# Performance work log

Measured on AMD Instinct MI355X. Metric: run time of the kernel, lower is better.

Reference implementation:

```python
import jax, jax.numpy as jnp
import numpy as np

NUM_NEIGHBORS = 9  # cfg['num_neighbors']


def _cdist(a, b):
    """Euclidean cdist. a: [..., M, D], b: [..., N, D] -> [..., M, N]."""
    a2 = jnp.sum(a * a, axis=-1)[..., :, None]
    b2 = jnp.sum(b * b, axis=-1)[..., None, :]
    ab = jnp.einsum('...md,...nd->...mn', a, b)
    return jnp.sqrt(jnp.maximum(a2 + b2 - 2.0 * ab, 0.0))


def setup_inputs() -> dict:
    key = jax.random.key(0)
    k1, k2 = jax.random.split(key)
    B, P, D, N = 8, 784, 384, 16384
    embedding = jax.random.normal(k1, (B * P, D), dtype=jnp.float32)
    embedding_coreset = jax.random.normal(k2, (N, D), dtype=jnp.float32)
    return {"embedding": embedding, "embedding_coreset": embedding_coreset, "batch_size": B}


def reference(embedding, embedding_coreset, batch_size):
    D = embedding.shape[-1]
    # 1-NN of every patch against the coreset
    dists = _cdist(embedding, embedding_coreset)          # [B*P, N]
    patch_scores = jnp.min(dists, axis=1).reshape(batch_size, -1)   # [B, P]
    locations = jnp.argmin(dists, axis=1).reshape(batch_size, -1)   # [B, P]

    b = jnp.arange(batch_size)
    max_patches = jnp.argmax(patch_scores, axis=1)        # [B]
    emb = embedding.reshape(batch_size, -1, D)            # [B, P, D]
    max_feats = emb[b, max_patches]                       # [B, D]
    score = patch_scores[b, max_patches]                  # [B]
    nn_index = locations[b, max_patches]                  # [B]
    nn_sample = embedding_coreset[nn_index]               # [B, D]

    # k-NN of the nearest coreset sample within the coreset (support set)
    d_nn = _cdist(nn_sample, embedding_coreset)           # [B, N]
    _, support = jax.lax.top_k(-d_nn, NUM_NEIGHBORS)      # smallest dists, ascending -> [B, K]
    support_feats = embedding_coreset[support]            # [B, K, D]

    # distances from max patch feature to the support samples
    d_sup = _cdist(max_feats[:, None, :], support_feats)[:, 0, :]  # [B, K]
    weights = (1.0 - jax.nn.softmax(d_sup, axis=1))[:, 0]          # [B]
    return weights * score
```

## Files before the change

kernel.cpp:

```cpp
#include <hip/hip_runtime.h>
#include <hip/hip_bf16.h>
#include <math.h>

#define M_TOTAL 6272
#define N_CS    16384
#define D_DIM   384
#define BATCH   8
#define P_PATCH 784
#define KNN     9

#define MTILES  (M_TOTAL / 128)
#define NTILES2 (N_CS / 256)

typedef _Float16 half8 __attribute__((ext_vector_type(8)));
typedef float    floatx4 __attribute__((ext_vector_type(4)));

__device__ __forceinline__ void async_copy16(const void* g, void* l) {
    __builtin_amdgcn_global_load_lds(
        (const __attribute__((address_space(1))) void*)g,
        (__attribute__((address_space(3))) void*)l, 16, 0, 0);
}

__global__ void convert_all_kernel(const float* __restrict__ emb,
                                   const float* __restrict__ cs,
                                   _Float16* __restrict__ embh,
                                   _Float16* __restrict__ csh,
                                   float* __restrict__ cnorm) {
    int w = threadIdx.x >> 6, lane = threadIdx.x & 63;
    int row = blockIdx.x * 4 + w;
    if (row >= N_CS + M_TOTAL) return;
    bool is_cs = row < N_CS;
    const float* r = (is_cs ? cs + (size_t)row * D_DIM
                            : emb + (size_t)(row - N_CS) * D_DIM) + lane * 6;
    float2 a = *(const float2*)r;
    float2 b = *(const float2*)(r + 2);
    float2 c = *(const float2*)(r + 4);
    union { _Float16 h[2]; unsigned u; } p0, p1, p2;
    p0.h[0] = (_Float16)a.x; p0.h[1] = (_Float16)a.y;
    p1.h[0] = (_Float16)b.x; p1.h[1] = (_Float16)b.y;
    p2.h[0] = (_Float16)c.x; p2.h[1] = (_Float16)c.y;
    unsigned* dst = (unsigned*)(is_cs ? csh + (size_t)row * D_DIM
                                      : embh + (size_t)(row - N_CS) * D_DIM) + lane * 3;
    dst[0] = p0.u; dst[1] = p1.u; dst[2] = p2.u;
    if (is_cs) {
        float s = a.x * a.x + a.y * a.y + b.x * b.x + b.y * b.y + c.x * c.x + c.y * c.y;
#pragma unroll
        for (int mk = 1; mk <= 32; mk <<= 1) s += __shfl_xor(s, mk, 64);
        if (lane == 0) cnorm[row] = s;
    }
}

__global__ __launch_bounds__(256, 2) void mindist_mfma_kernel(
    const _Float16* __restrict__ embh, const _Float16* __restrict__ csh,
    const float* __restrict__ cnorm,
    float* __restrict__ pvals, int* __restrict__ pidx) {
    __shared__ _Float16 As[128 * 64];
    __shared__ _Float16 Bs[256 * 64];

    const int tid  = threadIdx.x;
    const int lane = tid & 63;
    const int w    = tid >> 6;
    const int wr   = w >> 1, wc = w & 1;
    const int row0  = blockIdx.x * 128;
    const int cbase = blockIdx.y * 256;
    const int q   = lane >> 4;
    const int cl  = lane & 15;
    const int cl7 = cl & 7;

    floatx4 acc[4][8];
#pragma unroll
    for (int mi = 0; mi < 4; ++mi)
#pragma unroll
        for (int nj = 0; nj < 8; ++nj) acc[mi][nj] = (floatx4){0.f, 0.f, 0.f, 0.f};

    float cn_l[8];
#pragma unroll
    for (int nj = 0; nj < 8; ++nj)
        cn_l[nj] = cnorm[cbase + wc * 128 + nj * 16 + cl];

    const int sub = lane >> 3;
    const int gch = (lane & 7) ^ sub;
    const int kb  = gch * 8;

    for (int kk = 0; kk < D_DIM; kk += 64) {
        __syncthreads();
#pragma unroll
        for (int i = 0; i < 12; ++i) {
            int inst = w * 12 + i;
            if (inst < 16) {
                int r = inst * 8 + sub;
                async_copy16(embh + (size_t)(row0 + r) * D_DIM + kk + kb,
                             &As[inst * 512 + lane * 8]);
            } else {
                int blk = inst - 16;
                int r = blk * 8 + sub;
                async_copy16(csh + (size_t)(cbase + r) * D_DIM + kk + kb,
                             &Bs[blk * 512 + lane * 8]);
            }
        }
        __syncthreads();
#pragma unroll
        for (int ks = 0; ks < 64; ks += 32) {
            const int ks8 = ks >> 3;
            half8 af[4], bf[8];
#pragma unroll
            for (int mi = 0; mi < 4; ++mi)
                af[mi] = *(const half8*)&As[(wr * 64 + mi * 16 + cl) * 64
                                            + (((ks8 + q) ^ cl7) * 8)];
#pragma unroll
            for (int nj = 0; nj < 8; ++nj)
                bf[nj] = *(const half8*)&Bs[(wc * 128 + nj * 16 + cl) * 64
                                            + (((ks8 + q) ^ cl7) * 8)];
#pragma unroll
            for (int mi = 0; mi < 4; ++mi)
#pragma unroll
                for (int nj = 0; nj < 8; ++nj)
                    acc[mi][nj] = __builtin_amdgcn_mfma_f32_16x16x32_f16(
                        af[mi], bf[nj], acc[mi][nj], 0, 0, 0);
        }
    }

    __syncthreads();
    float* smv = (float*)As;
    int*   smi = (int*)(As + 512);

#pragma unroll
    for (int mi = 0; mi < 4; ++mi) {
#pragma unroll
        for (int r = 0; r < 4; ++r) {
            float v = 3.4e38f; int idx = 0x7fffffff;
#pragma unroll
            for (int nj = 0; nj < 8; ++nj) {
                float d = cn_l[nj] - 2.f * acc[mi][nj][r];
                int   c = cbase + wc * 128 + nj * 16 + cl;
                if (d < v) { v = d; idx = c; }
            }
#pragma unroll
            for (int mk = 1; mk <= 8; mk <<= 1) {
                float v2 = __shfl_xor(v, mk, 64);
                int   i2 = __shfl_xor(idx, mk, 64);
                if (v2 < v || (v2 == v && i2 < idx)) { v = v2; idx = i2; }
            }
            if (cl == 0) {
                int rl = wr * 64 + mi * 16 + q * 4 + r;
                smv[rl * 2 + wc] = v;
                smi[rl * 2 + wc] = idx;
            }
        }
    }
    __syncthreads();
    if (tid < 128) {
        float v = smv[tid * 2];      int i = smi[tid * 2];
        float v1 = smv[tid * 2 + 1]; int i1 = smi[tid * 2 + 1];
        if (v1 < v) { v = v1; i = i1; }
        pvals[(size_t)(row0 + tid) * NTILES2 + blockIdx.y] = v;
        pidx[(size_t)(row0 + tid) * NTILES2 + blockIdx.y]  = i;
    }
}

__global__ void reduce_rescore_kernel(const float* __restrict__ pvals,
                                      const int* __restrict__ pidx,
                                      const float* __restrict__ emb,
                                      const float* __restrict__ cs,
                                      float* __restrict__ scores,
                                      int* __restrict__ loc) {
    int w = threadIdx.x >> 6, lane = threadIdx.x & 63;
    int m = blockIdx.x * 4 + w;
    float v = pvals[(size_t)m * NTILES2 + lane];
    int   i = pidx[(size_t)m * NTILES2 + lane];
#pragma unroll
    for (int mk = 1; mk <= 32; mk <<= 1) {
        float v2 = __shfl_xor(v, mk, 64);
        int   i2 = __shfl_xor(i, mk, 64);
        if (v2 < v || (v2 == v && i2 < i)) { v = v2; i = i2; }
    }
    const float* a = emb + (size_t)m * D_DIM;
    const float* b = cs + (size_t)i * D_DIM;
    float s = 0.f;
#pragma unroll
    for (int t = 0; t < D_DIM / 64; ++t) {
        float d = a[lane + t * 64] - b[lane + t * 64];
        s += d * d;
    }
#pragma unroll
    for (int mk = 1; mk <= 32; mk <<= 1) s += __shfl_xor(s, mk, 64);
    if (lane == 0) { scores[m] = sqrtf(s); loc[m] = i; }
}

__global__ void argmax_kernel(const float* __restrict__ scores,
                              const int* __restrict__ loc,
                              float* __restrict__ bscore,
                              int* __restrict__ bnn, int* __restrict__ bpatch) {
    int b = blockIdx.x;
    int tid = threadIdx.x;
    float bv = -1.f;
    int bp = 0x7fffffff;
    for (int p = tid; p < P_PATCH; p += 256) {
        float v = scores[b * P_PATCH + p];
        if (v > bv || (v == bv && p < bp)) { bv = v; bp = p; }
    }
    __shared__ float sv[256];
    __shared__ int   sp[256];
    sv[tid] = bv; sp[tid] = bp;
    __syncthreads();
    for (int off = 128; off > 0; off >>= 1) {
        if (tid < off) {
            float v = sv[tid + off]; int p = sp[tid + off];
            if (v > sv[tid] || (v == sv[tid] && p < sp[tid])) { sv[tid] = v; sp[tid] = p; }
        }
        __syncthreads();
    }
    if (tid == 0) {
        bscore[b] = sv[0];
        bpatch[b] = sp[0];
        bnn[b]    = loc[b * P_PATCH + sp[0]];
    }
}

__global__ void dnn_kernel(const float* __restrict__ cs,
                           const float* __restrict__ cnorm,
                           const int* __restrict__ bnn,
                           float* __restrict__ dmat) {
    int lane = threadIdx.x & 63;
    int gw = (blockIdx.x * 256 + threadIdx.x) >> 6;
    float qv[BATCH][6];
#pragma unroll
    for (int b = 0; b < BATCH; ++b) {
        const float* qr = cs + (size_t)bnn[b] * D_DIM + lane * 6;
#pragma unroll
        for (int j = 0; j < 6; ++j) qv[b][j] = qr[j];
    }
    for (int n = gw; n < N_CS; n += 1024) {
        const float* r = cs + (size_t)n * D_DIM + lane * 6;
        float x[6];
#pragma unroll
        for (int j = 0; j < 6; ++j) x[j] = r[j];
        float s[BATCH];
#pragma unroll
        for (int b = 0; b < BATCH; ++b) {
            float t = 0.f;
#pragma unroll
            for (int j = 0; j < 6; ++j) t += x[j] * qv[b][j];
            s[b] = t;
        }
#pragma unroll
        for (int b = 0; b < BATCH; ++b)
#pragma unroll
            for (int mk = 1; mk <= 32; mk <<= 1) s[b] += __shfl_xor(s[b], mk, 64);
        if (lane < BATCH) {
            float sv = s[0];
#pragma unroll
            for (int b = 1; b < BATCH; ++b) sv = (lane == b) ? s[b] : sv;
            dmat[(size_t)lane * N_CS + n] = cnorm[n] - 2.f * sv;
        }
    }
}

__device__ inline void merge9(float* av, int* ai, const float* bv, const int* bi) {
    float mv[KNN]; int mi[KNN];
    int x = 0, y = 0;
#pragma unroll
    for (int k = 0; k < KNN; ++k) {
        bool ta = (av[x] < bv[y]) || (av[x] == bv[y] && ai[x] < bi[y]);
        if (ta) { mv[k] = av[x]; mi[k] = ai[x]; ++x; }
        else    { mv[k] = bv[y]; mi[k] = bi[y]; ++y; }
    }
#pragma unroll
    for (int k = 0; k < KNN; ++k) { av[k] = mv[k]; ai[k] = mi[k]; }
}

__global__ void top9_final_kernel(const float* __restrict__ dmat,
                                  const float* __restrict__ emb,
                                  const float* __restrict__ cs,
                                  const float* __restrict__ bscore,
                                  const int* __restrict__ bpatch,
                                  float* __restrict__ out) {
    int b = blockIdx.x;
    int tid = threadIdx.x;
    __shared__ float lv[512][KNN];
    __shared__ int   li[512][KNN];
    __shared__ float mf[D_DIM];
    __shared__ float dsup[KNN];

    int mp = bpatch[b];
    const float* frow = emb + (size_t)(b * P_PATCH + mp) * D_DIM;
    for (int i = tid; i < D_DIM; i += 512) mf[i] = frow[i];

    float tv[KNN]; int ti[KNN];
#pragma unroll
    for (int k = 0; k < KNN; ++k) { tv[k] = 3.4e38f; ti[k] = 0x7fffffff; }
    for (int n = tid; n < N_CS; n += 512) {
        float d = dmat[(size_t)b * N_CS + n];
        if (d < tv[KNN - 1] || (d == tv[KNN - 1] && n < ti[KNN - 1])) {
            tv[KNN - 1] = d; ti[KNN - 1] = n;
#pragma unroll
            for (int k = KNN - 1; k > 0; --k) {
                if (tv[k] < tv[k - 1] || (tv[k] == tv[k - 1] && ti[k] < ti[k - 1])) {
                    float fv = tv[k]; tv[k] = tv[k - 1]; tv[k - 1] = fv;
                    int   iv = ti[k]; ti[k] = ti[k - 1]; ti[k - 1] = iv;
                }
            }
        }
    }
#pragma unroll
    for (int k = 0; k < KNN; ++k) { lv[tid][k] = tv[k]; li[tid][k] = ti[k]; }
    __syncthreads();
    for (int off = 256; off > 0; off >>= 1) {
        if (tid < off) {
            float av[KNN]; int ai[KNN]; float bv2[KNN]; int bi2[KNN];
#pragma unroll
            for (int k = 0; k < KNN; ++k) {
                av[k]  = lv[tid][k];        ai[k]  = li[tid][k];
                bv2[k] = lv[tid + off][k];  bi2[k] = li[tid + off][k];
            }
            merge9(av, ai, bv2, bi2);
#pragma unroll
            for (int k = 0; k < KNN; ++k) { lv[tid][k] = av[k]; li[tid][k] = ai[k]; }
        }
        __syncthreads();
    }
    {
        int k      = tid >> 5;
        int lane32 = tid & 31;
        if (k < KNN) {
            int idx = li[0][k];
            const float* r = cs + (size_t)idx * D_DIM;
            float s = 0.f;
            for (int i = lane32; i < D_DIM; i += 32) {
                float df = mf[i] - r[i];
                s += df * df;
            }
#pragma unroll
            for (int mk = 1; mk <= 16; mk <<= 1) s += __shfl_xor(s, mk, 64);
            if (lane32 == 0) dsup[k] = sqrtf(fmaxf(s, 0.f));
        }
    }
    __syncthreads();
    if (tid == 0) {
        float mx = dsup[0];
        for (int k = 1; k < KNN; ++k) mx = fmaxf(mx, dsup[k]);
        float sum = 0.f, e0 = 0.f;
        for (int k = 0; k < KNN; ++k) {
            float e = expf(dsup[k] - mx);
            sum += e;
            if (k == 0) e0 = e;
        }
        out[b] = (1.f - e0 / sum) * bscore[b];
    }
}

extern "C" void kernel_launch(void* const* d_in, const int* in_sizes, int n_in,
                              void* d_out, int out_size, void* d_ws, size_t ws_size,
                              hipStream_t stream) {
    (void)in_sizes; (void)n_in; (void)out_size; (void)ws_size;
    const float* emb = (const float*)d_in[0];
    const float* cs  = (const float*)d_in[1];
    float* out = (float*)d_out;

    char* p = (char*)d_ws;
    float* cnorm  = (float*)p;  p += (size_t)N_CS * 4;
    float* pvals  = (float*)p;  p += (size_t)M_TOTAL * NTILES2 * 4;
    int*   pidx   = (int*)p;    p += (size_t)M_TOTAL * NTILES2 * 4;
    float* scores = (float*)p;  p += (size_t)M_TOTAL * 4;
    int*   loc    = (int*)p;    p += (size_t)M_TOTAL * 4;
    float* bscore = (float*)p;  p += BATCH * 4;
    int*   bpatch = (int*)p;    p += BATCH * 4;
    int*   bnn    = (int*)p;    p += BATCH * 4;
    float* dmat   = (float*)p;  p += (size_t)BATCH * N_CS * 4;
    p = (char*)(((size_t)p + 15) & ~(size_t)15);
    _Float16* embh = (_Float16*)p; p += (size_t)M_TOTAL * D_DIM * 2;
    _Float16* csh  = (_Float16*)p; p += (size_t)N_CS * D_DIM * 2;

    {
        int rows = N_CS + M_TOTAL;
        convert_all_kernel<<<(rows + 3) / 4, 256, 0, stream>>>(emb, cs, embh, csh, cnorm);
    }
    {
        dim3 grid(MTILES, NTILES2);
        mindist_mfma_kernel<<<grid, 256, 0, stream>>>(embh, csh, cnorm, pvals, pidx);
    }
    reduce_rescore_kernel<<<M_TOTAL / 4, 256, 0, stream>>>(pvals, pidx, emb, cs, scores, loc);
    argmax_kernel<<<BATCH, 256, 0, stream>>>(scores, loc, bscore, bnn, bpatch);
    dnn_kernel<<<256, 256, 0, stream>>>(cs, cnorm, bnn, dmat);
    top9_final_kernel<<<BATCH, 512, 0, stream>>>(dmat, emb, cs, bscore, bpatch, out);
}
```

Measured before the change: 306.7 us.

## Fuse argmax into rescore via packed atomicMax, swizzle GEMM grid, raise occupancy

Removes the separate per-batch argmax kernel. reduce_rescore now does an atomicMax on a packed 64-bit key (score bits high, inverted patch index low) per batch, and that key is zeroed in the convert kernel. The mindist GEMM moves to a 1D grid whose blockIdx is remapped so each group of 64 consecutive blocks covers one row tile and all 64 column tiles in a permuted order, which is meant to improve cache reuse. Its launch bounds also rise to 3 blocks per SM, which may cause register spills. The packed key relies on nonnegative scores ordering correctly as uint bits.

Result: slower. 829.5 us (+170.5%).

```diff
diff --git a/kernel.cpp b/kernel.cpp
--- a/kernel.cpp
+++ b/kernel.cpp
@@ -25,7 +25,9 @@
                                    const float* __restrict__ cs,
                                    _Float16* __restrict__ embh,
                                    _Float16* __restrict__ csh,
-                                   float* __restrict__ cnorm) {
+                                   float* __restrict__ cnorm,
+                                   unsigned long long* __restrict__ packed) {
+    if (blockIdx.x == 0 && threadIdx.x < BATCH) packed[threadIdx.x] = 0ull;
     int w = threadIdx.x >> 6, lane = threadIdx.x & 63;
     int row = blockIdx.x * 4 + w;
     if (row >= N_CS + M_TOTAL) return;
@@ -50,19 +52,22 @@
     }
 }
 
-__global__ __launch_bounds__(256, 2) void mindist_mfma_kernel(
+__global__ __launch_bounds__(256, 3) void mindist_mfma_kernel(
     const _Float16* __restrict__ embh, const _Float16* __restrict__ csh,
     const float* __restrict__ cnorm,
     float* __restrict__ pvals, int* __restrict__ pidx) {
     __shared__ _Float16 As[128 * 64];
     __shared__ _Float16 Bs[256 * 64];
 
+    const int b    = blockIdx.x;
+    const int bx   = b >> 6;
+    const int by   = ((b & 7) << 3) | ((b >> 3) & 7);
     const int tid  = threadIdx.x;
     const int lane = tid & 63;
     const int w    = tid >> 6;
     const int wr   = w >> 1, wc = w & 1;
-    const int row0  = blockIdx.x * 128;
-    const int cbase = blockIdx.y * 256;
+    const int row0  = bx * 128;
+    const int cbase = by * 256;
     const int q   = lane >> 4;
     const int cl  = lane & 15;
     const int cl7 = cl & 7;
@@ -153,8 +158,8 @@
         float v = smv[tid * 2];      int i = smi[tid * 2];
         float v1 = smv[tid * 2 + 1]; int i1 = smi[tid * 2 + 1];
         if (v1 < v) { v = v1; i = i1; }
-        pvals[(size_t)(row0 + tid) * NTILES2 + blockIdx.y] = v;
-        pidx[(size_t)(row0 + tid) * NTILES2 + blockIdx.y]  = i;
+        pvals[(size_t)(row0 + tid) * NTILES2 + by] = v;
+        pidx[(size_t)(row0 + tid) * NTILES2 + by]  = i;
     }
 }
 
@@ -163,7 +168,8 @@
                                       const float* __restrict__ emb,
                                       const float* __restrict__ cs,
                                       float* __restrict__ scores,
-                                      int* __restrict__ loc) {
+                                      int* __restrict__ loc,
+                                      unsigned long long* __restrict__ packed) {
     int w = threadIdx.x >> 6, lane = threadIdx.x & 63;
     int m = blockIdx.x * 4 + w;
     float v = pvals[(size_t)m * NTILES2 + lane];
@@ -184,49 +190,31 @@
     }
 #pragma unroll
     for (int mk = 1; mk <= 32; mk <<= 1) s += __shfl_xor(s, mk, 64);
-    if (lane == 0) { scores[m] = sqrtf(s); loc[m] = i; }
-}
-
-__global__ void argmax_kernel(const float* __restrict__ scores,
-                              const int* __restrict__ loc,
-                              float* __restrict__ bscore,
-                              int* __restrict__ bnn, int* __restrict__ bpatch) {
-    int b = blockIdx.x;
-    int tid = threadIdx.x;
-    float bv = -1.f;
-    int bp = 0x7fffffff;
-    for (int p = tid; p < P_PATCH; p += 256) {
-        float v = scores[b * P_PATCH + p];
-        if (v > bv || (v == bv && p < bp)) { bv = v; bp = p; }
-    }
-    __shared__ float sv[256];
-    __shared__ int   sp[256];
-    sv[tid] = bv; sp[tid] = bp;
-    __syncthreads();
-    for (int off = 128; off > 0; off >>= 1) {
-        if (tid < off) {
-            float v = sv[tid + off]; int p = sp[tid + off];
-            if (v > sv[tid] || (v == sv[tid] && p < sp[tid])) { sv[tid] = v; sp[tid] = p; }
-        }
-        __syncthreads();
-    }
-    if (tid == 0) {
-        bscore[b] = sv[0];
-        bpatch[b] = sp[0];
-        bnn[b]    = loc[b * P_PATCH + sp[0]];
+    if (lane == 0) {
+        float sc = sqrtf(s);
+        scores[m] = sc;
+        loc[m] = i;
+        int bb = m / P_PATCH, p = m % P_PATCH;
+        unsigned long long key =
+            ((unsigned long long)__float_as_uint(sc) << 32) |
+            (unsigned)(0x7fffffff - p);
+        atomicMax(&packed[bb], key);
     }
 }
 
 __global__ void dnn_kernel(const float* __restrict__ cs,
                            const float* __restrict__ cnorm,
-                           const int* __restrict__ bnn,
+                           const unsigned long long* __restrict__ packed,
+                           const int* __restrict__ loc,
                            float* __restrict__ dmat) {
     int lane = threadIdx.x & 63;
     int gw = (blockIdx.x * 256 + threadIdx.x) >> 6;
     float qv[BATCH][6];
 #pragma unroll
     for (int b = 0; b < BATCH; ++b) {
-        const float* qr = cs + (size_t)bnn[b] * D_DIM + lane * 6;
+        int p  = 0x7fffffff - (unsigned)(packed[b] & 0xffffffffull);
+        int nn = loc[b * P_PATCH + p];
+        const float* qr = cs + (size_t)nn * D_DIM + lane * 6;
 #pragma unroll
         for (int j = 0; j < 6; ++j) qv[b][j] = qr[j];
     }
@@ -272,8 +260,7 @@
 __global__ void top9_final_kernel(const float* __restrict__ dmat,
                                   const float* __restrict__ emb,
                                   const float* __restrict__ cs,
-                                  const float* __restrict__ bscore,
-                                  const int* __restrict__ bpatch,
+                                  const unsigned long long* __restrict__ packed,
                                   float* __restrict__ out) {
     int b = blockIdx.x;
     int tid = threadIdx.x;
@@ -282,7 +269,9 @@
     __shared__ float mf[D_DIM];
     __shared__ float dsup[KNN];
 
-    int mp = bpatch[b];
+    unsigned long long key = packed[b];
+    int   mp     = 0x7fffffff - (unsigned)(key & 0xffffffffull);
+    float bscore = __uint_as_float((unsigned)(key >> 32));
     const float* frow = emb + (size_t)(b * P_PATCH + mp) * D_DIM;
     for (int i = tid; i < D_DIM; i += 512) mf[i] = frow[i];
 
@@ -345,7 +334,7 @@
             sum += e;
             if (k == 0) e0 = e;
         }
-        out[b] = (1.f - e0 / sum) * bscore[b];
+        out[b] = (1.f - e0 / sum) * bscore;
     }
 }
 
@@ -363,9 +352,8 @@
     int*   pidx   = (int*)p;    p += (size_t)M_TOTAL * NTILES2 * 4;
     float* scores = (float*)p;  p += (size_t)M_TOTAL * 4;
     int*   loc    = (int*)p;    p += (size_t)M_TOTAL * 4;
-    float* bscore = (float*)p;  p += BATCH * 4;
-    int*   bpatch = (int*)p;    p += BATCH * 4;
-    int*   bnn    = (int*)p;    p += BATCH * 4;
+    p = (char*)(((size_t)p + 7) & ~(size_t)7);
+    unsigned long long* packed = (unsigned long long*)p; p += BATCH * 8;
     float* dmat   = (float*)p;  p += (size_t)BATCH * N_CS * 4;
     p = (char*)(((size_t)p + 15) & ~(size_t)15);
     _Float16* embh = (_Float16*)p; p += (size_t)M_TOTAL * D_DIM * 2;
@@ -373,14 +361,13 @@
 
     {
         int rows = N_CS + M_TOTAL;
-        convert_all_kernel<<<(rows + 3) / 4, 256, 0, stream>>>(emb, cs, embh, csh, cnorm);
-    }
-    {
-        dim3 grid(MTILES, NTILES2);
-        mindist_mfma_kernel<<<grid, 256, 0, stream>>>(embh, csh, cnorm, pvals, pidx);
-    }
-    reduce_rescore_kernel<<<M_TOTAL / 4, 256, 0, stream>>>(pvals, pidx, emb, cs, scores, loc);
-    argmax_kernel<<<BATCH, 256, 0, stream>>>(scores, loc, bscore, bnn, bpatch);
-    dnn_kernel<<<256, 256, 0, stream>>>(cs, cnorm, bnn, dmat);
-    top9_final_kernel<<<BATCH, 512, 0, stream>>>(dmat, emb, cs, bscore, bpatch, out);
-}
+        convert_all_kernel<<<(rows + 3) / 4, 256, 0, stream>>>(emb, cs, embh, csh,
+                                                               cnorm, packed);
+    }
+    mindist_mfma_kernel<<<MTILES * NTILES2, 256, 0, stream>>>(embh, csh, cnorm,
+                                                              pvals, pidx);
+    reduce_rescore_kernel<<<M_TOTAL / 4, 256, 0, stream>>>(pvals, pidx, emb, cs,
+                                                           scores, loc, packed);
+    dnn_kernel<<<256, 256, 0, stream>>>(cs, cnorm, packed, loc, dmat);
+    top9_final_kernel<<<BATCH, 512, 0, stream>>>(dmat, emb, cs, packed, out);
+}
```
